# Kernel tuning notes

Hardware: AMD Instinct MI355X
Metric: run time of the kernel (lower is better)

## Reference

```python
import jax, jax.numpy as jnp
import numpy as np

B, T, D = 32, 2048, 512

def setup_inputs() -> dict:
    key = jax.random.key(0)
    k1, k2, k3 = jax.random.split(key, 3)
    return {
        "query": jax.random.normal(k1, (B, D), dtype=jnp.float32),
        "key": jax.random.normal(k2, (B, T, D), dtype=jnp.float32),
        "value": jax.random.normal(k3, (B, T, D), dtype=jnp.float32),
    }

def reference(query, key, value):
    # energy: [B, T] = bmm(key [B,T,D], query [B,D,1]).squeeze
    energy = jnp.einsum("btd,bd->bt", key, query)
    attention = jax.nn.softmax(energy, axis=1)  # over T, no scaling/masking (faithful)
    # context: [B, D] = bmm(attention [B,1,T], value [B,T,D]).squeeze
    out = jnp.einsum("bt,btd->bd", attention, value)
    return (out, attention)
```

## Files before the change

### kernel.cpp

```cpp
#include <hip/hip_runtime.h>

#define B_ 32
#define T_ 2048
#define D_ 512

__global__ __launch_bounds__(256) void energy_kernel(
    const float* __restrict__ q,
    const float* __restrict__ key,
    float* __restrict__ energy)
{
    __shared__ float4 qs[128];
    const int b = blockIdx.x >> 9;
    if (threadIdx.x < 128)
        qs[threadIdx.x] = ((const float4*)q)[b * 128 + threadIdx.x];
    __syncthreads();

    const int wave = threadIdx.x >> 6;
    const int lane = threadIdx.x & 63;
    const int gw   = blockIdx.x * 4 + wave;
    const int t    = gw & (T_ - 1);

    const float4* k4 = (const float4*)key + (size_t)(b * T_ + t) * (D_ / 4);
    float acc = 0.f;
#pragma unroll
    for (int j = 0; j < 2; ++j) {
        float4 kv = k4[j * 64 + lane];
        float4 qv = qs[j * 64 + lane];
        acc += kv.x * qv.x + kv.y * qv.y + kv.z * qv.z + kv.w * qv.w;
    }
#pragma unroll
    for (int off = 32; off >= 1; off >>= 1)
        acc += __shfl_down(acc, off);
    if (lane == 0)
        energy[gw] = acc;
}

__global__ __launch_bounds__(256) void softmax_kernel(
    const float* __restrict__ energy,
    float* __restrict__ attn)
{
    const int b = blockIdx.x;
    const int wave = threadIdx.x >> 6;
    const int lane = threadIdx.x & 63;

    const float4* e4 = (const float4*)(energy + b * T_);
    float4 v0 = e4[threadIdx.x * 2 + 0];
    float4 v1 = e4[threadIdx.x * 2 + 1];

    float m = fmaxf(fmaxf(fmaxf(v0.x, v0.y), fmaxf(v0.z, v0.w)),
                    fmaxf(fmaxf(v1.x, v1.y), fmaxf(v1.z, v1.w)));
#pragma unroll
    for (int off = 32; off >= 1; off >>= 1)
        m = fmaxf(m, __shfl_xor(m, off));
    __shared__ float redm[4];
    if (lane == 0) redm[wave] = m;
    __syncthreads();
    m = fmaxf(fmaxf(redm[0], redm[1]), fmaxf(redm[2], redm[3]));

    float4 x0, x1;
    x0.x = expf(v0.x - m); x0.y = expf(v0.y - m);
    x0.z = expf(v0.z - m); x0.w = expf(v0.w - m);
    x1.x = expf(v1.x - m); x1.y = expf(v1.y - m);
    x1.z = expf(v1.z - m); x1.w = expf(v1.w - m);
    float s = x0.x + x0.y + x0.z + x0.w + x1.x + x1.y + x1.z + x1.w;
#pragma unroll
    for (int off = 32; off >= 1; off >>= 1)
        s += __shfl_xor(s, off);
    __shared__ float reds[4];
    if (lane == 0) reds[wave] = s;
    __syncthreads();
    s = reds[0] + reds[1] + reds[2] + reds[3];

    const float inv = 1.f / s;
    x0.x *= inv; x0.y *= inv; x0.z *= inv; x0.w *= inv;
    x1.x *= inv; x1.y *= inv; x1.z *= inv; x1.w *= inv;

    float4* a4 = (float4*)(attn + b * T_);
    a4[threadIdx.x * 2 + 0] = x0;
    a4[threadIdx.x * 2 + 1] = x1;
}

__global__ __launch_bounds__(512) void context_partial_kernel(
    const float* __restrict__ attn,
    const float* __restrict__ value,
    float* __restrict__ partial)
{
    __shared__ float  attn_s[256];
    __shared__ float4 red4[512];

    const int b     = blockIdx.x >> 3;
    const int chunk = blockIdx.x & 7;
    const int t0    = chunk * 256;

    if (threadIdx.x < 256)
        attn_s[threadIdx.x] = attn[b * T_ + t0 + threadIdx.x];
    __syncthreads();

    const int tg = threadIdx.x >> 7;
    const int d4 = threadIdx.x & 127;

    const float4* v4 = (const float4*)value + (size_t)(b * T_ + t0 + tg) * (D_ / 4) + d4;
    float4 acc = {0.f, 0.f, 0.f, 0.f};
#pragma unroll 8
    for (int i = 0; i < 64; ++i) {
        const float a = attn_s[4 * i + tg];
        const float4 vv = v4[i * 4 * (D_ / 4)];
        acc.x += a * vv.x; acc.y += a * vv.y;
        acc.z += a * vv.z; acc.w += a * vv.w;
    }

    red4[tg * 128 + d4] = acc;
    __syncthreads();
    if (threadIdx.x < 128) {
        float4 a0 = red4[threadIdx.x +   0];
        float4 a1 = red4[threadIdx.x + 128];
        float4 a2 = red4[threadIdx.x + 256];
        float4 a3 = red4[threadIdx.x + 384];
        float4 sv;
        sv.x = a0.x + a1.x + a2.x + a3.x;
        sv.y = a0.y + a1.y + a2.y + a3.y;
        sv.z = a0.z + a1.z + a2.z + a3.z;
        sv.w = a0.w + a1.w + a2.w + a3.w;
        ((float4*)partial)[(b * 8 + chunk) * 128 + threadIdx.x] = sv;
    }
}

__global__ __launch_bounds__(128) void reduce_kernel(
    const float* __restrict__ partial,
    float* __restrict__ out)
{
    const int b  = blockIdx.x;
    const int d4 = threadIdx.x;
    float4 s = {0.f, 0.f, 0.f, 0.f};
#pragma unroll
    for (int c = 0; c < 8; ++c) {
        float4 p = ((const float4*)partial)[(b * 8 + c) * 128 + d4];
        s.x += p.x; s.y += p.y; s.z += p.z; s.w += p.w;
    }
    ((float4*)out)[b * 128 + d4] = s;
}

extern "C" void kernel_launch(void* const* d_in, const int* in_sizes, int n_in,
                              void* d_out, int out_size, void* d_ws, size_t ws_size,
                              hipStream_t stream)
{
    const float* q     = (const float*)d_in[0];
    const float* key   = (const float*)d_in[1];
    const float* value = (const float*)d_in[2];

    float* out  = (float*)d_out;
    float* attn = out + B_ * D_;

    float* energy  = (float*)d_ws;
    float* partial = energy + B_ * T_;

    energy_kernel<<<B_ * T_ / 4, 256, 0, stream>>>(q, key, energy);
    softmax_kernel<<<B_, 256, 0, stream>>>(energy, attn);
    context_partial_kernel<<<B_ * 8, 512, 0, stream>>>(attn, value, partial);
    reduce_kernel<<<B_, 128, 0, stream>>>(partial, out);
}
```

Baseline: 276.8 us.

## Fuse softmax into context kernel and batch 8 rows per wave in energy

The energy kernel now has each wave compute 8 key rows. Query is held in registers instead of shared memory, and a transpose-style butterfly shuffle reduces all 8 dot products together, which removes the per-row full reductions and the block sync. The separate softmax kernel is gone: each context block recomputes the row max and sum from the energy vector and normalizes only its own 128-element slice. The context split doubles to 16 chunks per batch, giving 512 blocks. This trades redundant softmax reductions, repeated once per chunk, for one fewer launch and more parallelism in the value pass.

```diff
diff --git a/kernel.cpp b/kernel.cpp
--- a/kernel.cpp
+++ b/kernel.cpp
@@ -9,104 +9,115 @@
     const float* __restrict__ key,
     float* __restrict__ energy)
 {
-    __shared__ float4 qs[128];
-    const int b = blockIdx.x >> 9;
-    if (threadIdx.x < 128)
-        qs[threadIdx.x] = ((const float4*)q)[b * 128 + threadIdx.x];
-    __syncthreads();
-
+    const int b    = blockIdx.x >> 6;
+    const int blk  = blockIdx.x & 63;
     const int wave = threadIdx.x >> 6;
     const int lane = threadIdx.x & 63;
-    const int gw   = blockIdx.x * 4 + wave;
-    const int t    = gw & (T_ - 1);
+    const int t0   = blk * 32 + wave * 8;
 
-    const float4* k4 = (const float4*)key + (size_t)(b * T_ + t) * (D_ / 4);
-    float acc = 0.f;
+    const float4* q4 = (const float4*)q + b * 128;
+    const float4 qv0 = q4[lane];
+    const float4 qv1 = q4[64 + lane];
+
+    const float4* k4 = (const float4*)key + (size_t)(b * T_ + t0) * 128;
+
+    float a[8];
 #pragma unroll
-    for (int j = 0; j < 2; ++j) {
-        float4 kv = k4[j * 64 + lane];
-        float4 qv = qs[j * 64 + lane];
-        acc += kv.x * qv.x + kv.y * qv.y + kv.z * qv.z + kv.w * qv.w;
+    for (int r = 0; r < 8; ++r) {
+        const float4 k0 = k4[r * 128 + lane];
+        const float4 k1 = k4[r * 128 + 64 + lane];
+        a[r] = k0.x * qv0.x + k0.y * qv0.y + k0.z * qv0.z + k0.w * qv0.w
+             + k1.x * qv1.x + k1.y * qv1.y + k1.z * qv1.z + k1.w * qv1.w;
+    }
+
+#pragma unroll
+    for (int i = 0; i < 4; ++i) {
+        const float send = (lane & 1) ? a[2 * i] : a[2 * i + 1];
+        const float keep = (lane & 1) ? a[2 * i + 1] : a[2 * i];
+        a[i] = keep + __shfl_xor(send, 1);
     }
 #pragma unroll
-    for (int off = 32; off >= 1; off >>= 1)
-        acc += __shfl_down(acc, off);
-    if (lane == 0)
-        energy[gw] = acc;
+    for (int i = 0; i < 2; ++i) {
+        const float send = (lane & 2) ? a[2 * i] : a[2 * i + 1];
+        const float keep = (lane & 2) ? a[2 * i + 1] : a[2 * i];
+        a[i] = keep + __shfl_xor(send, 2);
+    }
+    {
+        const float send = (lane & 4) ? a[0] : a[1];
+        const float keep = (lane & 4) ? a[1] : a[0];
+        a[0] = keep + __shfl_xor(send, 4);
+    }
+    a[0] += __shfl_xor(a[0], 8);
+    a[0] += __shfl_xor(a[0], 16);
+    a[0] += __shfl_xor(a[0], 32);
+
+    if (lane < 8)
+        energy[b * T_ + t0 + lane] = a[0];
 }
 
-__global__ __launch_bounds__(256) void softmax_kernel(
+__global__ __launch_bounds__(512) void ctx_kernel(
     const float* __restrict__ energy,
-    float* __restrict__ attn)
+    const float* __restrict__ value,
+    float* __restrict__ attn,
+    float* __restrict__ partial)
 {
-    const int b = blockIdx.x;
-    const int wave = threadIdx.x >> 6;
-    const int lane = threadIdx.x & 63;
+    __shared__ float  red_m[8];
+    __shared__ float  red_s[8];
+    __shared__ float4 attn_s4[32];
+    __shared__ float4 red4[512];
+
+    const int b     = blockIdx.x >> 4;
+    const int chunk = blockIdx.x & 15;
+    const int t0    = chunk * 128;
+    const int wave  = threadIdx.x >> 6;
+    const int lane  = threadIdx.x & 63;
 
     const float4* e4 = (const float4*)(energy + b * T_);
-    float4 v0 = e4[threadIdx.x * 2 + 0];
-    float4 v1 = e4[threadIdx.x * 2 + 1];
-
-    float m = fmaxf(fmaxf(fmaxf(v0.x, v0.y), fmaxf(v0.z, v0.w)),
-                    fmaxf(fmaxf(v1.x, v1.y), fmaxf(v1.z, v1.w)));
+    const float4 ev  = e4[threadIdx.x];
+    float m = fmaxf(fmaxf(ev.x, ev.y), fmaxf(ev.z, ev.w));
 #pragma unroll
     for (int off = 32; off >= 1; off >>= 1)
         m = fmaxf(m, __shfl_xor(m, off));
-    __shared__ float redm[4];
-    if (lane == 0) redm[wave] = m;
+    if (lane == 0) red_m[wave] = m;
     __syncthreads();
-    m = fmaxf(fmaxf(redm[0], redm[1]), fmaxf(redm[2], redm[3]));
+    m = red_m[0];
+#pragma unroll
+    for (int w = 1; w < 8; ++w) m = fmaxf(m, red_m[w]);
 
-    float4 x0, x1;
-    x0.x = expf(v0.x - m); x0.y = expf(v0.y - m);
-    x0.z = expf(v0.z - m); x0.w = expf(v0.w - m);
-    x1.x = expf(v1.x - m); x1.y = expf(v1.y - m);
-    x1.z = expf(v1.z - m); x1.w = expf(v1.w - m);
-    float s = x0.x + x0.y + x0.z + x0.w + x1.x + x1.y + x1.z + x1.w;
+    float s = expf(ev.x - m) + expf(ev.y - m) + expf(ev.z - m) + expf(ev.w - m);
 #pragma unroll
     for (int off = 32; off >= 1; off >>= 1)
         s += __shfl_xor(s, off);
-    __shared__ float reds[4];
-    if (lane == 0) reds[wave] = s;
+    if (lane == 0) red_s[wave] = s;
     __syncthreads();
-    s = reds[0] + reds[1] + reds[2] + reds[3];
+    s = red_s[0] + red_s[1] + red_s[2] + red_s[3]
+      + red_s[4] + red_s[5] + red_s[6] + red_s[7];
+    const float inv = 1.f / s;
 
-    const float inv = 1.f / s;
-    x0.x *= inv; x0.y *= inv; x0.z *= inv; x0.w *= inv;
-    x1.x *= inv; x1.y *= inv; x1.z *= inv; x1.w *= inv;
-
-    float4* a4 = (float4*)(attn + b * T_);
-    a4[threadIdx.x * 2 + 0] = x0;
-    a4[threadIdx.x * 2 + 1] = x1;
-}
-
-__global__ __launch_bounds__(512) void context_partial_kernel(
-    const float* __restrict__ attn,
-    const float* __restrict__ value,
-    float* __restrict__ partial)
-{
-    __shared__ float  attn_s[256];
-    __shared__ float4 red4[512];
-
-    const int b     = blockIdx.x >> 3;
-    const int chunk = blockIdx.x & 7;
-    const int t0    = chunk * 256;
-
-    if (threadIdx.x < 256)
-        attn_s[threadIdx.x] = attn[b * T_ + t0 + threadIdx.x];
+    if (threadIdx.x < 32) {
+        const float4 ec = e4[chunk * 32 + threadIdx.x];
+        float4 p;
+        p.x = expf(ec.x - m) * inv;
+        p.y = expf(ec.y - m) * inv;
+        p.z = expf(ec.z - m) * inv;
+        p.w = expf(ec.w - m) * inv;
+        ((float4*)(attn + b * T_ + t0))[threadIdx.x] = p;
+        attn_s4[threadIdx.x] = p;
+    }
     __syncthreads();
 
     const int tg = threadIdx.x >> 7;
     const int d4 = threadIdx.x & 127;
+    const float* attn_s = (const float*)attn_s4;
 
-    const float4* v4 = (const float4*)value + (size_t)(b * T_ + t0 + tg) * (D_ / 4) + d4;
+    const float4* v4 = (const float4*)value + (size_t)(b * T_ + t0 + tg) * 128 + d4;
     float4 acc = {0.f, 0.f, 0.f, 0.f};
 #pragma unroll 8
-    for (int i = 0; i < 64; ++i) {
-        const float a = attn_s[4 * i + tg];
+    for (int i = 0; i < 32; ++i) {
+        const float aw  = attn_s[4 * i + tg];
         const float4 vv = v4[i * 4 * (D_ / 4)];
-        acc.x += a * vv.x; acc.y += a * vv.y;
-        acc.z += a * vv.z; acc.w += a * vv.w;
+        acc.x += aw * vv.x; acc.y += aw * vv.y;
+        acc.z += aw * vv.z; acc.w += aw * vv.w;
     }
 
     red4[tg * 128 + d4] = acc;
@@ -121,7 +132,7 @@
         sv.y = a0.y + a1.y + a2.y + a3.y;
         sv.z = a0.z + a1.z + a2.z + a3.z;
         sv.w = a0.w + a1.w + a2.w + a3.w;
-        ((float4*)partial)[(b * 8 + chunk) * 128 + threadIdx.x] = sv;
+        ((float4*)partial)[(b * 16 + chunk) * 128 + threadIdx.x] = sv;
     }
 }
 
@@ -133,8 +144,8 @@
     const int d4 = threadIdx.x;
     float4 s = {0.f, 0.f, 0.f, 0.f};
 #pragma unroll
-    for (int c = 0; c < 8; ++c) {
-        float4 p = ((const float4*)partial)[(b * 8 + c) * 128 + d4];
+    for (int c = 0; c < 16; ++c) {
+        float4 p = ((const float4*)partial)[(b * 16 + c) * 128 + d4];
         s.x += p.x; s.y += p.y; s.z += p.z; s.w += p.w;
     }
     ((float4*)out)[b * 128 + d4] = s;
@@ -154,8 +165,7 @@
     float* energy  = (float*)d_ws;
     float* partial = energy + B_ * T_;
 
-    energy_kernel<<<B_ * T_ / 4, 256, 0, stream>>>(q, key, energy);
-    softmax_kernel<<<B_, 256, 0, stream>>>(energy, attn);
-    context_partial_kernel<<<B_ * 8, 512, 0, stream>>>(attn, value, partial);
+    energy_kernel<<<B_ * 64, 256, 0, stream>>>(q, key, energy);
+    ctx_kernel<<<B_ * 16, 512, 0, stream>>>(energy, value, attn, partial);
     reduce_kernel<<<B_, 128, 0, stream>>>(partial, out);
 }
```

New measurement: 277.3 us. No clear change (+0.2%).
